# Kernel tuning notes

Hardware: AMD Instinct MI355X
Metric: run time of the kernel (lower is better)

The kernel has to match this reference:

```python
import jax, jax.numpy as jnp
import numpy as np

EPS = 1e-5  # batchnorm eps (torch default)


def setup_inputs() -> dict:
    key = jax.random.key(0)
    ks = jax.random.split(key, 16)
    N, E, Din, H, Dout = 100000, 600000, 128, 128, 64
    x = jax.random.normal(ks[0], (N, Din), dtype=jnp.float32)
    edge_index = jax.random.randint(ks[1], (2, E), 0, N, dtype=jnp.int64)
    def lin(k, fan_in, fan_out):
        s = 1.0 / np.sqrt(fan_in)
        return jax.random.uniform(k, (fan_in, fan_out), jnp.float32, -s, s)
    return {
        "x": x,
        "edge_index": edge_index,
        "W1": lin(ks[2], Din, H), "b1": jnp.zeros((H,), jnp.float32),
        "W2": lin(ks[3], H, H),   "b2": jnp.zeros((H,), jnp.float32),
        "W3": lin(ks[4], H, H),   "b3": jnp.zeros((H,), jnp.float32),
        "W4": lin(ks[5], H, Dout),"b4": jnp.zeros((Dout,), jnp.float32),
        "g1": jnp.ones((H,), jnp.float32), "be1": jnp.zeros((H,), jnp.float32),
        "g2": jnp.ones((H,), jnp.float32), "be2": jnp.zeros((H,), jnp.float32),
        "g3": jnp.ones((H,), jnp.float32), "be3": jnp.zeros((H,), jnp.float32),
    }


def _gcn_norm(edge_index, N, dtype):
    # GCNConv default: add self-loops, symmetric normalization D^-1/2 A D^-1/2
    loop = jnp.arange(N, dtype=edge_index.dtype)
    src = jnp.concatenate([edge_index[0], loop])
    dst = jnp.concatenate([edge_index[1], loop])
    deg = jax.ops.segment_sum(jnp.ones_like(src, dtype=dtype), dst, num_segments=N)
    dinv = jax.lax.rsqrt(deg)  # deg >= 1 thanks to self-loops
    norm = dinv[src] * dinv[dst]  # [E+N]
    return src, dst, norm


def _conv(h, W, b, src, dst, norm, N):
    hw = h @ W                      # [N, out]
    msg = hw[src] * norm[:, None]   # gather + scale, [E+N, out]
    return jax.ops.segment_sum(msg, dst, num_segments=N) + b


def _bn(h, gamma, beta):
    # training-mode batchnorm over node dimension (biased variance)
    mu = jnp.mean(h, axis=0)
    var = jnp.mean(jnp.square(h - mu), axis=0)
    return (h - mu) * jax.lax.rsqrt(var + EPS) * gamma + beta


def reference(x, edge_index, W1, b1, W2, b2, W3, b3, W4, b4,
              g1, be1, g2, be2, g3, be3):
    N = x.shape[0]
    src, dst, norm = _gcn_norm(edge_index, N, x.dtype)
    h = jax.nn.relu(_conv(x, W1, b1, src, dst, norm, N))
    h = _bn(h, g1, be1)
    h = jax.nn.relu(_conv(h, W2, b2, src, dst, norm, N))
    h = _bn(h, g2, be2)
    h = jax.nn.relu(_conv(h, W3, b3, src, dst, norm, N))
    h = _bn(h, g3, be3)
    h = jax.nn.relu(_conv(h, W4, b4, src, dst, norm, N))
    return h
```

## Files before the change

### kernel.cpp

```cpp
#include <hip/hip_runtime.h>

#define BN_EPS 1e-5f

using bfrag = __attribute__((ext_vector_type(8))) short;
using f32x4 = __attribute__((ext_vector_type(4))) float;

__device__ inline float bf2f(unsigned int h16) {
    union { unsigned int u; float f; } v; v.u = h16 << 16; return v.f;
}
__device__ inline unsigned short f2bf(float f) {
    union { float f; unsigned int u; } v; v.f = f;
    unsigned int u = v.u;
    u += 0x7fffu + ((u >> 16) & 1u);
    return (unsigned short)(u >> 16);
}
__device__ inline void unpack8(uint4 u, float* f) {
    f[0] = bf2f(u.x & 0xffffu); f[1] = bf2f(u.x >> 16);
    f[2] = bf2f(u.y & 0xffffu); f[3] = bf2f(u.y >> 16);
    f[4] = bf2f(u.z & 0xffffu); f[5] = bf2f(u.z >> 16);
    f[6] = bf2f(u.w & 0xffffu); f[7] = bf2f(u.w >> 16);
}
__device__ inline void fma8(uint4 G, float w, float* acc) {
    float v[8];
    unpack8(G, v);
#pragma unroll
    for (int k = 0; k < 8; ++k) acc[k] += w * v[k];
}


__global__ void count_kernel(const int* __restrict__ ei, int E, int* __restrict__ cnt) {
    int e = blockIdx.x * blockDim.x + threadIdx.x;
    if (e < E) atomicAdd(&cnt[ei[E + e]], 1);
}

__global__ void dinv_kernel(const int* __restrict__ cnt, float* __restrict__ dinv, int N) {
    int i = blockIdx.x * blockDim.x + threadIdx.x;
    if (i < N) dinv[i] = rsqrtf((float)(cnt[i] + 1));
}

__global__ __launch_bounds__(1024) void scan_blocks(const int* __restrict__ cnt,
                                                    int* __restrict__ rowptr,
                                                    int* __restrict__ bsum, int N) {
    __shared__ int sh[1024];
    int t = threadIdx.x;
    int i = blockIdx.x * 1024 + t;
    int v = (i < N) ? cnt[i] + 1 : 0;
    sh[t] = v;
    __syncthreads();
    for (int off = 1; off < 1024; off <<= 1) {
        int x = (t >= off) ? sh[t - off] : 0;
        __syncthreads();
        sh[t] += x;
        __syncthreads();
    }
    if (i < N) rowptr[i] = sh[t] - v;
    if (t == 1023) bsum[blockIdx.x] = sh[1023];
}

__global__ void scan_carry(const int* __restrict__ bsum, int* __restrict__ boff, int nblk) {
    if (threadIdx.x == 0 && blockIdx.x == 0) {
        int run = 0;
        for (int b = 0; b < nblk; ++b) { int v = bsum[b]; boff[b] = run; run += v; }
        boff[nblk] = run;
    }
}

__global__ void scan_add(int* __restrict__ rowptr, const int* __restrict__ boff,
                         int* __restrict__ cursor, int N, int nblk) {
    int i = blockIdx.x * blockDim.x + threadIdx.x;
    if (i < N) {
        int v = rowptr[i] + boff[i >> 10];
        rowptr[i] = v;
        cursor[i] = v;
    }
    if (i == 0) rowptr[N] = boff[nblk];
}

__global__ void fill_kernel(const int* __restrict__ ei, int E, int* __restrict__ cursor,
                            const float* __restrict__ dinv, int2* __restrict__ epack) {
    int e = blockIdx.x * blockDim.x + threadIdx.x;
    if (e < E) {
        int s = ei[e], d = ei[E + e];
        int p = atomicAdd(&cursor[d], 1);
        float nrm = dinv[s] * dinv[d];
        epack[p] = make_int2(s, __float_as_int(nrm));
    }
}

__global__ void self_kernel(int N, int* __restrict__ cursor, const float* __restrict__ dinv,
                            int2* __restrict__ epack) {
    int i = blockIdx.x * blockDim.x + threadIdx.x;
    if (i < N) {
        int p = atomicAdd(&cursor[i], 1);
        float w = dinv[i] * dinv[i];
        epack[p] = make_int2(i, __float_as_int(w));
    }
}

__global__ void s_kernel(const int* __restrict__ rowptr, const int2* __restrict__ epack,
                         float* __restrict__ sarr, int N) {
    int i = blockIdx.x * blockDim.x + threadIdx.x;
    if (i < N) {
        float a = 0.f;
        int j1 = rowptr[i + 1];
        for (int j = rowptr[i]; j < j1; ++j) a += __int_as_float(epack[j].y);
        sarr[i] = a;
    }
}


template <bool HASBN>
__global__ __launch_bounds__(256) void prep_kernel(const float* __restrict__ W, int COLS,
                                                   const float* __restrict__ stats,
                                                   const float* __restrict__ g,
                                                   const float* __restrict__ be, float invN,
                                                   unsigned short* __restrict__ Wt,
                                                   float* __restrict__ cvec) {
    __shared__ float sc[128], sh[128];
    int tid = threadIdx.x;
    if (tid < 128) {
        if (HASBN) {
            float mu  = stats[tid] * invN;
            float var = stats[128 + tid] * invN - mu * mu;
            float rs  = rsqrtf(var + BN_EPS);
            float s   = rs * g[tid];
            sc[tid] = s;
            sh[tid] = be[tid] - mu * s;
        } else { sc[tid] = 1.f; sh[tid] = 0.f; }
    }
    __syncthreads();
    int total = 128 * COLS;
    for (int idx = blockIdx.x * 256 + tid; idx < total; idx += gridDim.x * 256) {
        int k = idx / COLS, j = idx % COLS;
        Wt[j * 128 + k] = f2bf(sc[k] * W[idx]);
    }
    if (blockIdx.x == 0 && tid < COLS) {
        float a = 0.f;
        if (HASBN)
            for (int k = 0; k < 128; ++k) a += sh[k] * W[k * COLS + tid];
        cvec[tid] = a;
    }
}


template <int COLS, bool IN_F32>
__global__ __launch_bounds__(256) void gemm_mfma(const void* __restrict__ Hin,
                                                 const unsigned short* __restrict__ Wt,
                                                 unsigned short* __restrict__ out, int N) {
    __shared__ unsigned short Hs[64][136];
    const int tid  = threadIdx.x;
    const int row0 = blockIdx.x * 64;

    if (IN_F32) {
        const float* H = (const float*)Hin;
#pragma unroll
        for (int it = 0; it < 8; ++it) {
            int idx = it * 256 + tid;
            int r = idx >> 5, c4 = (idx & 31) * 4;
            float4 v = {0.f, 0.f, 0.f, 0.f};
            if (row0 + r < N) v = *(const float4*)(H + (size_t)(row0 + r) * 128 + c4);
            Hs[r][c4 + 0] = f2bf(v.x); Hs[r][c4 + 1] = f2bf(v.y);
            Hs[r][c4 + 2] = f2bf(v.z); Hs[r][c4 + 3] = f2bf(v.w);
        }
    } else {
        const unsigned short* H = (const unsigned short*)Hin;
#pragma unroll
        for (int it = 0; it < 4; ++it) {
            int idx = it * 256 + tid;
            int r = idx >> 4, c8 = (idx & 15) * 8;
            uint4 v = {0u, 0u, 0u, 0u};
            if (row0 + r < N) v = *(const uint4*)(H + (size_t)(row0 + r) * 128 + c8);
            *(uint4*)&Hs[r][c8] = v;
        }
    }
    __syncthreads();

    const int lane = tid & 63, wave = tid >> 6;
    const int arow = lane & 15, kg = lane >> 4;
    const int r0   = wave * 16;

    bfrag af[4];
#pragma unroll
    for (int kc = 0; kc < 4; ++kc) af[kc] = *(const bfrag*)&Hs[r0 + arow][kc * 32 + kg * 8];

    constexpr int NT = COLS / 16;
    f32x4 acc[NT];
#pragma unroll
    for (int nt = 0; nt < NT; ++nt) acc[nt] = (f32x4){0.f, 0.f, 0.f, 0.f};

#pragma unroll
    for (int nt = 0; nt < NT; ++nt) {
        const unsigned short* wp = Wt + (size_t)(nt * 16 + arow) * 128 + kg * 8;
#pragma unroll
        for (int kc = 0; kc < 4; ++kc) {
            bfrag bf = *(const bfrag*)(wp + kc * 32);
            acc[nt] = __builtin_amdgcn_mfma_f32_16x16x32_bf16(af[kc], bf, acc[nt], 0, 0, 0);
        }
    }
    __syncthreads();

#pragma unroll
    for (int nt = 0; nt < NT; ++nt) {
        int col = nt * 16 + arow;
#pragma unroll
        for (int r = 0; r < 4; ++r)
            Hs[r0 + kg * 4 + r][col] = f2bf(acc[nt][r]);
    }
    __syncthreads();

    constexpr int CH = COLS / 8;
    for (int idx = tid; idx < 64 * CH; idx += 256) {
        int r = idx / CH, c8 = (idx % CH) * 8;
        if (row0 + r < N)
            *(uint4*)(out + (size_t)(row0 + r) * COLS + c8) = *(const uint4*)&Hs[r][c8];
    }
}


template <int F, bool STATS, bool HASC, typename TOUT, int RG>
__global__ __launch_bounds__(256) void agg_kernel(const unsigned short* __restrict__ HW,
                                                  const int* __restrict__ rowptr,
                                                  const int2* __restrict__ epack,
                                                  const float* __restrict__ sarr,
                                                  const float* __restrict__ cvec,
                                                  const float* __restrict__ bias,
                                                  TOUT* __restrict__ out,
                                                  float* __restrict__ stats, int N) {
    constexpr int TPR  = F / 8;
    constexpr int NGRP = 256 / TPR;
    const int tid = threadIdx.x;
    const int grp = tid / TPR;
    const int j8  = (tid % TPR) * 8;
    const int r0  = (blockIdx.x * NGRP + grp) * RG;

    float ssum[8], ssq[8];
    if (STATS) {
#pragma unroll
        for (int k = 0; k < 8; ++k) { ssum[k] = 0.f; ssq[k] = 0.f; }
    }

    if (r0 < N) {
        float b8[8], c8[8];
#pragma unroll
        for (int k = 0; k < 8; ++k) b8[k] = bias[j8 + k];
        if (HASC) {
#pragma unroll
            for (int k = 0; k < 8; ++k) c8[k] = cvec[j8 + k];
        }

        const int e0 = rowptr[r0];
        int bound = rowptr[min(r0 + 1, N)];
        int bnd2  = rowptr[min(r0 + 2, N)];
        int bnd3  = rowptr[min(r0 + 3, N)];
        int bnd4  = rowptr[min(r0 + 4, N)];
        const int eend = bnd4;
        float sv = 0.f, sv2 = 0.f, sv3 = 0.f, sv4 = 0.f;
        if (HASC) {
            sv  = sarr[r0];
            sv2 = sarr[min(r0 + 1, N - 1)];
            sv3 = sarr[min(r0 + 2, N - 1)];
            sv4 = sarr[min(r0 + 3, N - 1)];
        }
        int r = r0;

        float acc[8];
#pragma unroll
        for (int k = 0; k < 8; ++k) acc[k] = 0.f;

#define FLUSH()                                                               \
    do {                                                                      \
        if (HASC) {                                                           \
            _Pragma("unroll") for (int k = 0; k < 8; ++k) acc[k] += c8[k] * sv; \
        }                                                                     \
        _Pragma("unroll") for (int k = 0; k < 8; ++k)                         \
            acc[k] = fmaxf(acc[k] + b8[k], 0.f);                              \
        if constexpr (sizeof(TOUT) == 2) {                                    \
            unsigned int p0 = (unsigned int)f2bf(acc[0]) | ((unsigned int)f2bf(acc[1]) << 16); \
            unsigned int p1 = (unsigned int)f2bf(acc[2]) | ((unsigned int)f2bf(acc[3]) << 16); \
            unsigned int p2 = (unsigned int)f2bf(acc[4]) | ((unsigned int)f2bf(acc[5]) << 16); \
            unsigned int p3 = (unsigned int)f2bf(acc[6]) | ((unsigned int)f2bf(acc[7]) << 16); \
            uint4 o = {p0, p1, p2, p3};                                       \
            *(uint4*)((unsigned short*)out + (size_t)r * F + j8) = o;         \
        } else {                                                              \
            float4 o0 = {acc[0], acc[1], acc[2], acc[3]};                     \
            float4 o1 = {acc[4], acc[5], acc[6], acc[7]};                     \
            *(float4*)((float*)out + (size_t)r * F + j8)     = o0;            \
            *(float4*)((float*)out + (size_t)r * F + j8 + 4) = o1;            \
        }                                                                     \
        if (STATS) {                                                          \
            _Pragma("unroll") for (int k = 0; k < 8; ++k) {                   \
                ssum[k] += acc[k];                                            \
                ssq[k]  += acc[k] * acc[k];                                   \
            }                                                                 \
        }                                                                     \
        _Pragma("unroll") for (int k = 0; k < 8; ++k) acc[k] = 0.f;           \
        sv = sv2; sv2 = sv3; sv3 = sv4;                                       \
        bound = bnd2; bnd2 = bnd3; bnd3 = bnd4;                               \
    } while (0)

#define EPLOAD(ss, ww, ii)                                                    \
    do { int _i = (ii);                                                       \
        if (_i < eend) { int2 _e = epack[_i];                                 \
            ss = _e.x; ww = __int_as_float(_e.y); }                           \
    } while (0)

#define GISS(G, gw, ss, ww)                                                   \
    do { G = *(const uint4*)(HW + (size_t)(ss) * F + j8); gw = (ww); } while (0)

#define CONS1(G, gw, ii)                                                      \
    do { int _c = (ii);                                                       \
        if (_c < eend) {                                                      \
            if (_c >= bound) { FLUSH(); ++r; }                                \
            fma8(G, gw, acc);                                                 \
        }                                                                     \
    } while (0)

        int sA0 = 0, sA1 = 0, sA2 = 0, sA3 = 0, sB0 = 0, sB1 = 0, sB2 = 0, sB3 = 0;
        float wA0 = 0, wA1 = 0, wA2 = 0, wA3 = 0, wB0 = 0, wB1 = 0, wB2 = 0, wB3 = 0;
        uint4 GA0 = {}, GA1 = {}, GA2 = {}, GA3 = {}, GB0 = {}, GB1 = {}, GB2 = {}, GB3 = {};
        float ga0 = 0, ga1 = 0, ga2 = 0, ga3 = 0, gb0 = 0, gb1 = 0, gb2 = 0, gb3 = 0;

        EPLOAD(sA0, wA0, e0 + 0); EPLOAD(sA1, wA1, e0 + 1);
        EPLOAD(sA2, wA2, e0 + 2); EPLOAD(sA3, wA3, e0 + 3);
        EPLOAD(sB0, wB0, e0 + 4); EPLOAD(sB1, wB1, e0 + 5);
        EPLOAD(sB2, wB2, e0 + 6); EPLOAD(sB3, wB3, e0 + 7);
        GISS(GA0, ga0, sA0, wA0); GISS(GA1, ga1, sA1, wA1);
        GISS(GA2, ga2, sA2, wA2); GISS(GA3, ga3, sA3, wA3);

        for (int b = e0; b < eend; b += 8) {
            EPLOAD(sA0, wA0, b + 8);  EPLOAD(sA1, wA1, b + 9);
            EPLOAD(sA2, wA2, b + 10); EPLOAD(sA3, wA3, b + 11);
            GISS(GB0, gb0, sB0, wB0); GISS(GB1, gb1, sB1, wB1);
            GISS(GB2, gb2, sB2, wB2); GISS(GB3, gb3, sB3, wB3);
            CONS1(GA0, ga0, b + 0); CONS1(GA1, ga1, b + 1);
            CONS1(GA2, ga2, b + 2); CONS1(GA3, ga3, b + 3);

            EPLOAD(sB0, wB0, b + 12); EPLOAD(sB1, wB1, b + 13);
            EPLOAD(sB2, wB2, b + 14); EPLOAD(sB3, wB3, b + 15);
            GISS(GA0, ga0, sA0, wA0); GISS(GA1, ga1, sA1, wA1);
            GISS(GA2, ga2, sA2, wA2); GISS(GA3, ga3, sA3, wA3);
            CONS1(GB0, gb0, b + 4); CONS1(GB1, gb1, b + 5);
            CONS1(GB2, gb2, b + 6); CONS1(GB3, gb3, b + 7);
        }
        FLUSH();

#undef FLUSH
#undef EPLOAD
#undef GISS
#undef CONS1
    }

    if constexpr (STATS) {
        __shared__ float red[NGRP][F];
#pragma unroll
        for (int k = 0; k < 8; ++k) red[grp][j8 + k] = ssum[k];
        __syncthreads();
        if (tid < F) {
            float a = 0.f;
#pragma unroll
            for (int g = 0; g < NGRP; ++g) a += red[g][tid];
            atomicAdd(&stats[tid], a);
        }
        __syncthreads();
#pragma unroll
        for (int k = 0; k < 8; ++k) red[grp][j8 + k] = ssq[k];
        __syncthreads();
        if (tid < F) {
            float a = 0.f;
#pragma unroll
            for (int g = 0; g < NGRP; ++g) a += red[g][tid];
            atomicAdd(&stats[F + tid], a);
        }
    }
}


extern "C" void kernel_launch(void* const* d_in, const int* in_sizes, int n_in,
                              void* d_out, int out_size, void* d_ws, size_t ws_size,
                              hipStream_t stream) {
    const float* x  = (const float*)d_in[0];
    const int*   ei = (const int*)d_in[1];
    const float* W1 = (const float*)d_in[2];  const float* b1 = (const float*)d_in[3];
    const float* W2 = (const float*)d_in[4];  const float* b2 = (const float*)d_in[5];
    const float* W3 = (const float*)d_in[6];  const float* b3 = (const float*)d_in[7];
    const float* W4 = (const float*)d_in[8];  const float* b4 = (const float*)d_in[9];
    const float* g1 = (const float*)d_in[10]; const float* be1 = (const float*)d_in[11];
    const float* g2 = (const float*)d_in[12]; const float* be2 = (const float*)d_in[13];
    const float* g3 = (const float*)d_in[14]; const float* be3 = (const float*)d_in[15];

    const int N = in_sizes[0] / 128;
    const int E = in_sizes[1] / 2;
    const int nblk = (N + 1023) / 1024;

    size_t off = 0;
    char* ws = (char*)d_ws;
    auto alloc = [&](size_t bytes) -> void* {
        void* p = ws + off;
        off += (bytes + 255) & ~(size_t)255;
        return p;
    };
    int*   cnt    = (int*)alloc((size_t)N * 4);
    float* dinv   = (float*)alloc((size_t)N * 4);
    int*   rowptr = (int*)alloc((size_t)(N + 1) * 4);
    int*   cursor = (int*)alloc((size_t)N * 4);
    int*   bsum   = (int*)alloc((size_t)nblk * 4);
    int*   boff   = (int*)alloc((size_t)(nblk + 1) * 4);
    int2*  epack  = (int2*)alloc((size_t)(E + N) * 8);
    float* sarr   = (float*)alloc((size_t)N * 4);
    float* stats  = (float*)alloc(256 * 4);
    unsigned short* Wt = (unsigned short*)alloc(128 * 128 * 2);
    float* cvec   = (float*)alloc(128 * 4);
    unsigned short* hA  = (unsigned short*)alloc((size_t)N * 128 * 2);
    unsigned short* hwB = (unsigned short*)alloc((size_t)N * 128 * 2);
    (void)ws_size; (void)n_in; (void)out_size;

    const int TB = 256;
    const int gE = (E + TB - 1) / TB;
    const int gN = (N + TB - 1) / TB;

    hipMemsetAsync(cnt, 0, (size_t)N * 4, stream);
    count_kernel<<<gE, TB, 0, stream>>>(ei, E, cnt);
    dinv_kernel<<<gN, TB, 0, stream>>>(cnt, dinv, N);
    scan_blocks<<<nblk, 1024, 0, stream>>>(cnt, rowptr, bsum, N);
    scan_carry<<<1, 1, 0, stream>>>(bsum, boff, nblk);
    scan_add<<<gN, TB, 0, stream>>>(rowptr, boff, cursor, N, nblk);
    fill_kernel<<<gE, TB, 0, stream>>>(ei, E, cursor, dinv, epack);
    self_kernel<<<gN, TB, 0, stream>>>(N, cursor, dinv, epack);
    s_kernel<<<gN, TB, 0, stream>>>(rowptr, epack, sarr, N);

    const int gG    = (N + 63) / 64;
    const int gA128 = (N + 63) / 64;
    const int gA64  = (N + 127) / 128;
    const float invN = 1.0f / (float)N;

    prep_kernel<false><<<8, 256, 0, stream>>>(W1, 128, nullptr, nullptr, nullptr, 0.f, Wt, cvec);
    gemm_mfma<128, true><<<gG, 256, 0, stream>>>(x, Wt, hwB, N);
    hipMemsetAsync(stats, 0, 256 * 4, stream);
    agg_kernel<128, true, false, unsigned short, 4><<<gA128, 256, 0, stream>>>(
        hwB, rowptr, epack, sarr, cvec, b1, hA, stats, N);

    prep_kernel<true><<<8, 256, 0, stream>>>(W2, 128, stats, g1, be1, invN, Wt, cvec);
    gemm_mfma<128, false><<<gG, 256, 0, stream>>>(hA, Wt, hwB, N);
    hipMemsetAsync(stats, 0, 256 * 4, stream);
    agg_kernel<128, true, true, unsigned short, 4><<<gA128, 256, 0, stream>>>(
        hwB, rowptr, epack, sarr, cvec, b2, hA, stats, N);

    prep_kernel<true><<<8, 256, 0, stream>>>(W3, 128, stats, g2, be2, invN, Wt, cvec);
    gemm_mfma<128, false><<<gG, 256, 0, stream>>>(hA, Wt, hwB, N);
    hipMemsetAsync(stats, 0, 256 * 4, stream);
    agg_kernel<128, true, true, unsigned short, 4><<<gA128, 256, 0, stream>>>(
        hwB, rowptr, epack, sarr, cvec, b3, hA, stats, N);

    prep_kernel<true><<<8, 256, 0, stream>>>(W4, 64, stats, g3, be3, invN, Wt, cvec);
    gemm_mfma<64, false><<<gG, 256, 0, stream>>>(hA, Wt, hwB, N);
    agg_kernel<64, false, true, float, 4><<<gA64, 256, 0, stream>>>(
        hwB, rowptr, epack, sarr, cvec, b4, (float*)d_out, nullptr, N);
}
```

Measured before the change: 461.3 us.

## Fold BN shift and bias into aggregation as virtual table rows; split stats pass

Appends two virtual rows to the HW table (BN shift vector c and bias) and adds two extra edges per node pointing at them, so the aggregation kernel no longer applies c*s and bias separately. sarr is now built with float atomics during fill, which removes s_kernel. BN statistics move out of the aggregation kernel into a separate stats pass that rereads hA, and the aggregation kernel gets a tighter launch bound. This adds extra gathers per node, stores c and bias in bf16 with some precision loss, and costs an extra full read of the activations per layer.

```diff
diff --git a/kernel.cpp b/kernel.cpp
--- a/kernel.cpp
+++ b/kernel.cpp
@@ -33,9 +33,14 @@
     if (e < E) atomicAdd(&cnt[ei[E + e]], 1);
 }
 
-__global__ void dinv_kernel(const int* __restrict__ cnt, float* __restrict__ dinv, int N) {
+__global__ void dinv_kernel(const int* __restrict__ cnt, float* __restrict__ dinv,
+                            float* __restrict__ sarr, int N) {
     int i = blockIdx.x * blockDim.x + threadIdx.x;
-    if (i < N) dinv[i] = rsqrtf((float)(cnt[i] + 1));
+    if (i < N) {
+        float d = rsqrtf((float)(cnt[i] + 1));
+        dinv[i] = d;
+        sarr[i] = d * d;
+    }
 }
 
 __global__ __launch_bounds__(1024) void scan_blocks(const int* __restrict__ cnt,
@@ -44,7 +49,7 @@
     __shared__ int sh[1024];
     int t = threadIdx.x;
     int i = blockIdx.x * 1024 + t;
-    int v = (i < N) ? cnt[i] + 1 : 0;
+    int v = (i < N) ? cnt[i] + 3 : 0;
     sh[t] = v;
     __syncthreads();
     for (int off = 1; off < 1024; off <<= 1) {
@@ -77,34 +82,27 @@
 }
 
 __global__ void fill_kernel(const int* __restrict__ ei, int E, int* __restrict__ cursor,
-                            const float* __restrict__ dinv, int2* __restrict__ epack) {
+                            const float* __restrict__ dinv, int2* __restrict__ epack,
+                            float* __restrict__ sarr) {
     int e = blockIdx.x * blockDim.x + threadIdx.x;
     if (e < E) {
         int s = ei[e], d = ei[E + e];
         int p = atomicAdd(&cursor[d], 1);
         float nrm = dinv[s] * dinv[d];
         epack[p] = make_int2(s, __float_as_int(nrm));
+        atomicAdd(&sarr[d], nrm);
     }
 }
 
 __global__ void self_kernel(int N, int* __restrict__ cursor, const float* __restrict__ dinv,
-                            int2* __restrict__ epack) {
+                            const float* __restrict__ sarr, int2* __restrict__ epack) {
     int i = blockIdx.x * blockDim.x + threadIdx.x;
     if (i < N) {
-        int p = atomicAdd(&cursor[i], 1);
-        float w = dinv[i] * dinv[i];
-        epack[p] = make_int2(i, __float_as_int(w));
-    }
-}
-
-__global__ void s_kernel(const int* __restrict__ rowptr, const int2* __restrict__ epack,
-                         float* __restrict__ sarr, int N) {
-    int i = blockIdx.x * blockDim.x + threadIdx.x;
-    if (i < N) {
-        float a = 0.f;
-        int j1 = rowptr[i + 1];
-        for (int j = rowptr[i]; j < j1; ++j) a += __int_as_float(epack[j].y);
-        sarr[i] = a;
+        int p = atomicAdd(&cursor[i], 3);
+        float d = dinv[i];
+        epack[p]     = make_int2(i, __float_as_int(d * d));
+        epack[p + 1] = make_int2(N, __float_as_int(sarr[i]));
+        epack[p + 2] = make_int2(N + 1, __float_as_int(1.0f));
     }
 }
 
@@ -114,8 +112,9 @@
                                                    const float* __restrict__ stats,
                                                    const float* __restrict__ g,
                                                    const float* __restrict__ be, float invN,
+                                                   const float* __restrict__ bias,
                                                    unsigned short* __restrict__ Wt,
-                                                   float* __restrict__ cvec) {
+                                                   unsigned short* __restrict__ table, int N) {
     __shared__ float sc[128], sh[128];
     int tid = threadIdx.x;
     if (tid < 128) {
@@ -138,7 +137,8 @@
         float a = 0.f;
         if (HASBN)
             for (int k = 0; k < 128; ++k) a += sh[k] * W[k * COLS + tid];
-        cvec[tid] = a;
+        table[(size_t)N * COLS + tid]       = f2bf(a);
+        table[(size_t)(N + 1) * COLS + tid] = f2bf(bias[tid]);
     }
 }
 
@@ -217,63 +217,73 @@
 }
 
 
-template <int F, bool STATS, bool HASC, typename TOUT, int RG>
-__global__ __launch_bounds__(256) void agg_kernel(const unsigned short* __restrict__ HW,
-                                                  const int* __restrict__ rowptr,
-                                                  const int2* __restrict__ epack,
-                                                  const float* __restrict__ sarr,
-                                                  const float* __restrict__ cvec,
-                                                  const float* __restrict__ bias,
-                                                  TOUT* __restrict__ out,
-                                                  float* __restrict__ stats, int N) {
+__global__ __launch_bounds__(256) void stats_kernel(const unsigned short* __restrict__ y,
+                                                    float* __restrict__ stats, int N) {
+    const int tid = threadIdx.x;
+    const int j8  = (tid & 15) * 8;
+    const int lr  = tid >> 4;
+    float ssum[8], ssq[8];
+#pragma unroll
+    for (int k = 0; k < 8; ++k) { ssum[k] = 0.f; ssq[k] = 0.f; }
+    for (int row = blockIdx.x * 16 + lr; row < N; row += gridDim.x * 16) {
+        uint4 u = *(const uint4*)(y + (size_t)row * 128 + j8);
+        float v[8];
+        unpack8(u, v);
+#pragma unroll
+        for (int k = 0; k < 8; ++k) { ssum[k] += v[k]; ssq[k] += v[k] * v[k]; }
+    }
+    __shared__ float red[16][128];
+#pragma unroll
+    for (int k = 0; k < 8; ++k) red[lr][j8 + k] = ssum[k];
+    __syncthreads();
+    if (tid < 128) {
+        float a = 0.f;
+#pragma unroll
+        for (int g = 0; g < 16; ++g) a += red[g][tid];
+        atomicAdd(&stats[tid], a);
+    }
+    __syncthreads();
+#pragma unroll
+    for (int k = 0; k < 8; ++k) red[lr][j8 + k] = ssq[k];
+    __syncthreads();
+    if (tid < 128) {
+        float a = 0.f;
+#pragma unroll
+        for (int g = 0; g < 16; ++g) a += red[g][tid];
+        atomicAdd(&stats[128 + tid], a);
+    }
+}
+
+
+template <int F, typename TOUT>
+__global__ __launch_bounds__(256, 8) void agg_kernel(const unsigned short* __restrict__ HW,
+                                                     const int* __restrict__ rowptr,
+                                                     const int2* __restrict__ epack,
+                                                     TOUT* __restrict__ out, int N) {
     constexpr int TPR  = F / 8;
     constexpr int NGRP = 256 / TPR;
     const int tid = threadIdx.x;
     const int grp = tid / TPR;
     const int j8  = (tid % TPR) * 8;
-    const int r0  = (blockIdx.x * NGRP + grp) * RG;
-
-    float ssum[8], ssq[8];
-    if (STATS) {
-#pragma unroll
-        for (int k = 0; k < 8; ++k) { ssum[k] = 0.f; ssq[k] = 0.f; }
-    }
-
-    if (r0 < N) {
-        float b8[8], c8[8];
-#pragma unroll
-        for (int k = 0; k < 8; ++k) b8[k] = bias[j8 + k];
-        if (HASC) {
-#pragma unroll
-            for (int k = 0; k < 8; ++k) c8[k] = cvec[j8 + k];
-        }
-
-        const int e0 = rowptr[r0];
-        int bound = rowptr[min(r0 + 1, N)];
-        int bnd2  = rowptr[min(r0 + 2, N)];
-        int bnd3  = rowptr[min(r0 + 3, N)];
-        int bnd4  = rowptr[min(r0 + 4, N)];
-        const int eend = bnd4;
-        float sv = 0.f, sv2 = 0.f, sv3 = 0.f, sv4 = 0.f;
-        if (HASC) {
-            sv  = sarr[r0];
-            sv2 = sarr[min(r0 + 1, N - 1)];
-            sv3 = sarr[min(r0 + 2, N - 1)];
-            sv4 = sarr[min(r0 + 3, N - 1)];
-        }
-        int r = r0;
-
-        float acc[8];
-#pragma unroll
-        for (int k = 0; k < 8; ++k) acc[k] = 0.f;
+    const int r0  = (blockIdx.x * NGRP + grp) * 4;
+    if (r0 >= N) return;
+
+    const int e0 = rowptr[r0];
+    int bound = rowptr[min(r0 + 1, N)];
+    int bnd2  = rowptr[min(r0 + 2, N)];
+    int bnd3  = rowptr[min(r0 + 3, N)];
+    int bnd4  = rowptr[min(r0 + 4, N)];
+    const int eend = bnd4;
+    int r = r0;
+
+    float acc[8];
+#pragma unroll
+    for (int k = 0; k < 8; ++k) acc[k] = 0.f;
 
 #define FLUSH()                                                               \
     do {                                                                      \
-        if (HASC) {                                                           \
-            _Pragma("unroll") for (int k = 0; k < 8; ++k) acc[k] += c8[k] * sv; \
-        }                                                                     \
         _Pragma("unroll") for (int k = 0; k < 8; ++k)                         \
-            acc[k] = fmaxf(acc[k] + b8[k], 0.f);                              \
+            acc[k] = fmaxf(acc[k], 0.f);                                      \
         if constexpr (sizeof(TOUT) == 2) {                                    \
             unsigned int p0 = (unsigned int)f2bf(acc[0]) | ((unsigned int)f2bf(acc[1]) << 16); \
             unsigned int p1 = (unsigned int)f2bf(acc[2]) | ((unsigned int)f2bf(acc[3]) << 16); \
@@ -287,14 +297,7 @@
             *(float4*)((float*)out + (size_t)r * F + j8)     = o0;            \
             *(float4*)((float*)out + (size_t)r * F + j8 + 4) = o1;            \
         }                                                                     \
-        if (STATS) {                                                          \
-            _Pragma("unroll") for (int k = 0; k < 8; ++k) {                   \
-                ssum[k] += acc[k];                                            \
-                ssq[k]  += acc[k] * acc[k];                                   \
-            }                                                                 \
-        }                                                                     \
         _Pragma("unroll") for (int k = 0; k < 8; ++k) acc[k] = 0.f;           \
-        sv = sv2; sv2 = sv3; sv3 = sv4;                                       \
         bound = bnd2; bnd2 = bnd3; bnd3 = bnd4;                               \
     } while (0)
 
@@ -315,63 +318,39 @@
         }                                                                     \
     } while (0)
 
-        int sA0 = 0, sA1 = 0, sA2 = 0, sA3 = 0, sB0 = 0, sB1 = 0, sB2 = 0, sB3 = 0;
-        float wA0 = 0, wA1 = 0, wA2 = 0, wA3 = 0, wB0 = 0, wB1 = 0, wB2 = 0, wB3 = 0;
-        uint4 GA0 = {}, GA1 = {}, GA2 = {}, GA3 = {}, GB0 = {}, GB1 = {}, GB2 = {}, GB3 = {};
-        float ga0 = 0, ga1 = 0, ga2 = 0, ga3 = 0, gb0 = 0, gb1 = 0, gb2 = 0, gb3 = 0;
-
-        EPLOAD(sA0, wA0, e0 + 0); EPLOAD(sA1, wA1, e0 + 1);
-        EPLOAD(sA2, wA2, e0 + 2); EPLOAD(sA3, wA3, e0 + 3);
-        EPLOAD(sB0, wB0, e0 + 4); EPLOAD(sB1, wB1, e0 + 5);
-        EPLOAD(sB2, wB2, e0 + 6); EPLOAD(sB3, wB3, e0 + 7);
+    int sA0 = 0, sA1 = 0, sA2 = 0, sA3 = 0, sB0 = 0, sB1 = 0, sB2 = 0, sB3 = 0;
+    float wA0 = 0, wA1 = 0, wA2 = 0, wA3 = 0, wB0 = 0, wB1 = 0, wB2 = 0, wB3 = 0;
+    uint4 GA0 = {}, GA1 = {}, GA2 = {}, GA3 = {}, GB0 = {}, GB1 = {}, GB2 = {}, GB3 = {};
+    float ga0 = 0, ga1 = 0, ga2 = 0, ga3 = 0, gb0 = 0, gb1 = 0, gb2 = 0, gb3 = 0;
+
+    EPLOAD(sA0, wA0, e0 + 0); EPLOAD(sA1, wA1, e0 + 1);
+    EPLOAD(sA2, wA2, e0 + 2); EPLOAD(sA3, wA3, e0 + 3);
+    EPLOAD(sB0, wB0, e0 + 4); EPLOAD(sB1, wB1, e0 + 5);
+    EPLOAD(sB2, wB2, e0 + 6); EPLOAD(sB3, wB3, e0 + 7);
+    GISS(GA0, ga0, sA0, wA0); GISS(GA1, ga1, sA1, wA1);
+    GISS(GA2, ga2, sA2, wA2); GISS(GA3, ga3, sA3, wA3);
+
+    for (int b = e0; b < eend; b += 8) {
+        EPLOAD(sA0, wA0, b + 8);  EPLOAD(sA1, wA1, b + 9);
+        EPLOAD(sA2, wA2, b + 10); EPLOAD(sA3, wA3, b + 11);
+        GISS(GB0, gb0, sB0, wB0); GISS(GB1, gb1, sB1, wB1);
+        GISS(GB2, gb2, sB2, wB2); GISS(GB3, gb3, sB3, wB3);
+        CONS1(GA0, ga0, b + 0); CONS1(GA1, ga1, b + 1);
+        CONS1(GA2, ga2, b + 2); CONS1(GA3, ga3, b + 3);
+
+        EPLOAD(sB0, wB0, b + 12); EPLOAD(sB1, wB1, b + 13);
+        EPLOAD(sB2, wB2, b + 14); EPLOAD(sB3, wB3, b + 15);
         GISS(GA0, ga0, sA0, wA0); GISS(GA1, ga1, sA1, wA1);
         GISS(GA2, ga2, sA2, wA2); GISS(GA3, ga3, sA3, wA3);
-
-        for (int b = e0; b < eend; b += 8) {
-            EPLOAD(sA0, wA0, b + 8);  EPLOAD(sA1, wA1, b + 9);
-            EPLOAD(sA2, wA2, b + 10); EPLOAD(sA3, wA3, b + 11);
-            GISS(GB0, gb0, sB0, wB0); GISS(GB1, gb1, sB1, wB1);
-            GISS(GB2, gb2, sB2, wB2); GISS(GB3, gb3, sB3, wB3);
-            CONS1(GA0, ga0, b + 0); CONS1(GA1, ga1, b + 1);
-            CONS1(GA2, ga2, b + 2); CONS1(GA3, ga3, b + 3);
-
-            EPLOAD(sB0, wB0, b + 12); EPLOAD(sB1, wB1, b + 13);
-            EPLOAD(sB2, wB2, b + 14); EPLOAD(sB3, wB3, b + 15);
-            GISS(GA0, ga0, sA0, wA0); GISS(GA1, ga1, sA1, wA1);
-            GISS(GA2, ga2, sA2, wA2); GISS(GA3, ga3, sA3, wA3);
-            CONS1(GB0, gb0, b + 4); CONS1(GB1, gb1, b + 5);
-            CONS1(GB2, gb2, b + 6); CONS1(GB3, gb3, b + 7);
-        }
-        FLUSH();
+        CONS1(GB0, gb0, b + 4); CONS1(GB1, gb1, b + 5);
+        CONS1(GB2, gb2, b + 6); CONS1(GB3, gb3, b + 7);
+    }
+    FLUSH();
 
 #undef FLUSH
 #undef EPLOAD
 #undef GISS
 #undef CONS1
-    }
-
-    if constexpr (STATS) {
-        __shared__ float red[NGRP][F];
-#pragma unroll
-        for (int k = 0; k < 8; ++k) red[grp][j8 + k] = ssum[k];
-        __syncthreads();
-        if (tid < F) {
-            float a = 0.f;
-#pragma unroll
-            for (int g = 0; g < NGRP; ++g) a += red[g][tid];
-            atomicAdd(&stats[tid], a);
-        }
-        __syncthreads();
-#pragma unroll
-        for (int k = 0; k < 8; ++k) red[grp][j8 + k] = ssq[k];
-        __syncthreads();
-        if (tid < F) {
-            float a = 0.f;
-#pragma unroll
-            for (int g = 0; g < NGRP; ++g) a += red[g][tid];
-            atomicAdd(&stats[F + tid], a);
-        }
-    }
 }
 
 
@@ -405,13 +384,12 @@
     int*   cursor = (int*)alloc((size_t)N * 4);
     int*   bsum   = (int*)alloc((size_t)nblk * 4);
     int*   boff   = (int*)alloc((size_t)(nblk + 1) * 4);
-    int2*  epack  = (int2*)alloc((size_t)(E + N) * 8);
+    int2*  epack  = (int2*)alloc((size_t)(E + 3 * (size_t)N) * 8);
     float* sarr   = (float*)alloc((size_t)N * 4);
     float* stats  = (float*)alloc(256 * 4);
-    unsigned short* Wt = (unsigned short*)alloc(128 * 128 * 2);
-    float* cvec   = (float*)alloc(128 * 4);
+    unsigned short* Wt  = (unsigned short*)alloc(128 * 128 * 2);
     unsigned short* hA  = (unsigned short*)alloc((size_t)N * 128 * 2);
-    unsigned short* hwB = (unsigned short*)alloc((size_t)N * 128 * 2);
+    unsigned short* hwB = (unsigned short*)alloc((size_t)(N + 2) * 128 * 2);
     (void)ws_size; (void)n_in; (void)out_size;
 
     const int TB = 256;
@@ -420,39 +398,38 @@
 
     hipMemsetAsync(cnt, 0, (size_t)N * 4, stream);
     count_kernel<<<gE, TB, 0, stream>>>(ei, E, cnt);
-    dinv_kernel<<<gN, TB, 0, stream>>>(cnt, dinv, N);
+    dinv_kernel<<<gN, TB, 0, stream>>>(cnt, dinv, sarr, N);
     scan_blocks<<<nblk, 1024, 0, stream>>>(cnt, rowptr, bsum, N);
     scan_carry<<<1, 1, 0, stream>>>(bsum, boff, nblk);
     scan_add<<<gN, TB, 0, stream>>>(rowptr, boff, cursor, N, nblk);
-    fill_kernel<<<gE, TB, 0, stream>>>(ei, E, cursor, dinv, epack);
-    self_kernel<<<gN, TB, 0, stream>>>(N, cursor, dinv, epack);
-    s_kernel<<<gN, TB, 0, stream>>>(rowptr, epack, sarr, N);
+    fill_kernel<<<gE, TB, 0, stream>>>(ei, E, cursor, dinv, epack, sarr);
+    self_kernel<<<gN, TB, 0, stream>>>(N, cursor, dinv, sarr, epack);
 
     const int gG    = (N + 63) / 64;
     const int gA128 = (N + 63) / 64;
     const int gA64  = (N + 127) / 128;
+    const int gS    = 1024;
     const float invN = 1.0f / (float)N;
 
-    prep_kernel<false><<<8, 256, 0, stream>>>(W1, 128, nullptr, nullptr, nullptr, 0.f, Wt, cvec);
+    prep_kernel<false><<<16, 256, 0, stream>>>(W1, 128, nullptr, nullptr, nullptr, 0.f, b1, Wt, hwB, N);
     gemm_mfma<128, true><<<gG, 256, 0, stream>>>(x, Wt, hwB, N);
+    agg_kernel<128, unsigned short><<<gA128, 256, 0, stream>>>(hwB, rowptr, epack, hA, N);
     hipMemsetAsync(stats, 0, 256 * 4, stream);
-    agg_kernel<128, true, false, unsigned short, 4><<<gA128, 256, 0, stream>>>(
-        hwB, rowptr, epack, sarr, cvec, b1, hA, stats, N);
-
-    prep_kernel<true><<<8, 256, 0, stream>>>(W2, 128, stats, g1, be1, invN, Wt, cvec);
+    stats_kernel<<<gS, 256, 0, stream>>>(hA, stats, N);
+
+    prep_kernel<true><<<16, 256, 0, stream>>>(W2, 128, stats, g1, be1, invN, b2, Wt, hwB, N);
     gemm_mfma<128, false><<<gG, 256, 0, stream>>>(hA, Wt, hwB, N);
+    agg_kernel<128, unsigned short><<<gA128, 256, 0, stream>>>(hwB, rowptr, epack, hA, N);
     hipMemsetAsync(stats, 0, 256 * 4, stream);
-    agg_kernel<128, true, true, unsigned short, 4><<<gA128, 256, 0, stream>>>(
-        hwB, rowptr, epack, sarr, cvec, b2, hA, stats, N);
-
-    prep_kernel<true><<<8, 256, 0, stream>>>(W3, 128, stats, g2, be2, invN, Wt, cvec);
+    stats_kernel<<<gS, 256, 0, stream>>>(hA, stats, N);
+
+    prep_kernel<true><<<16, 256, 0, stream>>>(W3, 128, stats, g2, be2, invN, b3, Wt, hwB, N);
     gemm_mfma<128, false><<<gG, 256, 0, stream>>>(hA, Wt, hwB, N);
+    agg_kernel<128, unsigned short><<<gA128, 256, 0, stream>>>(hwB, rowptr, epack, hA, N);
     hipMemsetAsync(stats, 0, 256 * 4, stream);
-    agg_kernel<128, true, true, unsigned short, 4><<<gA128, 256, 0, stream>>>(
-        hwB, rowptr, epack, sarr, cvec, b3, hA, stats, N);
-
-    prep_kernel<true><<<8, 256, 0, stream>>>(W4, 64, stats, g3, be3, invN, Wt, cvec);
+    stats_kernel<<<gS, 256, 0, stream>>>(hA, stats, N);
+
+    prep_kernel<true><<<16, 256, 0, stream>>>(W4, 64, stats, g3, be3, invN, b4, Wt, hwB, N);
     gemm_mfma<64, false><<<gG, 256, 0, stream>>>(hA, Wt, hwB, N);
-    agg_kernel<64, false, true, float, 4><<<gA64, 256, 0, stream>>>(
-        hwB, rowptr, epack, sarr, cvec, b4, (float*)d_out, nullptr, N);
-}
+    agg_kernel<64, float><<<gA64, 256, 0, stream>>>(hwB, rowptr, epack, (float*)d_out, N);
+}
```

Result: slower. 937.4 us (+103.2%).
